# Performance work log

Measured on AMD Instinct MI355X. Metric: run time of the kernel, lower is better.

The kernel has to match this reference:

```python
import jax, jax.numpy as jnp
import numpy as np
from jax import lax

BETA = 0.5
ITERATIONS = 20
EPS = 1e-12


def setup_inputs() -> dict:
    key = jax.random.key(0)
    n, K = 32768, 512
    # C plays the role of a cosine-similarity matrix; randn keeps exp(C/beta) bounded.
    C = jax.random.normal(key, (n, K), dtype=jnp.float32)
    return {"C": C}


def reference(C):
    n, K = C.shape
    a = jnp.float32(1.0 / n)          # uniform row marginal (scalar broadcast of a = ones(n,1)/n)
    b = jnp.float32(1.0 / K)          # uniform column marginal
    K_mat = jnp.exp(C / BETA)         # [n, K]
    Q0 = jnp.full((n, K), 1.0 / (n * K), dtype=C.dtype)
    sigma0 = jnp.full((K,), 1.0 / K, dtype=C.dtype)

    def step(carry, _):
        Q, sigma = carry
        Q = K_mat * sigma[None, :]                              # elementwise column scaling
        Q = Q / (jnp.sum(Q, axis=1, keepdims=True) + EPS) * a   # row-normalize to marginal a
        sigma = b / (jnp.sum(Q, axis=0) + EPS)                  # column sums (== Q^T @ ones)
        return (Q, sigma), None

    (Q, sigma), _ = lax.scan(step, (Q0, sigma0), None, length=ITERATIONS)
    return Q * n
```

## Files before the change

kernel.cpp:

```cpp
#include <hip/hip_runtime.h>
#include <cmath>


namespace {
constexpr int ROWS = 32768;
constexpr int COLS = 512;
constexpr int ITERS = 20;
constexpr float EPS = 1e-12f;
constexpr float A_M = 1.0f / 32768.0f;
constexpr float B_M = 1.0f / 512.0f;
constexpr float L2E2 = 2.8853900817779268f;
constexpr int NSH = 8;
constexpr int SLAB_ROWS = ROWS / 8;
constexpr int GSIG_OFF = 0;
constexpr int TSUM_OFF = ITERS * COLS;
constexpr int FLAG_OFF = TSUM_OFF + (ITERS - 1) * NSH * COLS;
constexpr size_t KB_BYTES = (size_t)ROWS * COLS * 2;
constexpr size_t CTRL_FLOATS = (size_t)FLAG_OFF + 512;
constexpr int PBLK = 512;
constexpr int PRPW = 8;
constexpr int WPB = 4;
constexpr int MID_BLOCKS = 1024;
constexpr int MID_RPW = 8;
constexpr int BIG_BLOCKS = 2048;
constexpr int BIG_RPW = 4;

typedef float f4v __attribute__((ext_vector_type(4)));
}

__device__ __forceinline__ float bflo(unsigned u) {
  union { unsigned i; float f; } v; v.i = u << 16; return v.f;
}
__device__ __forceinline__ float bfhi(unsigned u) {
  union { unsigned i; float f; } v; v.i = u & 0xFFFF0000u; return v.f;
}
__device__ __forceinline__ unsigned f2bf(float f) {
  union { float f; unsigned u; } v; v.f = f;
  return (v.u + 0x7FFFu + ((v.u >> 16) & 1u)) >> 16;
}
__device__ __forceinline__ int row_base_mid(int bid, int wave) {
  return (bid & 7) * SLAB_ROWS + ((bid >> 3) * WPB + wave) * MID_RPW;
}
__device__ __forceinline__ int row_base_big(int bid, int wave) {
  return (bid & 7) * SLAB_ROWS + ((bid >> 3) * WPB + wave) * BIG_RPW;
}

__global__ __launch_bounds__(256) void ipot_zero_kernel(float* __restrict__ ctrl) {
  const size_t stride = (size_t)gridDim.x * blockDim.x;
  const size_t gtid = (size_t)blockIdx.x * blockDim.x + threadIdx.x;
  if (gtid < COLS) ctrl[GSIG_OFF + gtid] = B_M;
  const size_t zsz = (size_t)(ITERS - 1) * NSH * COLS + 512;
  for (size_t i = gtid; i < zsz; i += stride) ctrl[TSUM_OFF + i] = 0.0f;
}

__global__ __launch_bounds__(512, 4) void ipot_persist_kernel(
    const float* __restrict__ C, float* __restrict__ out,
    float* __restrict__ ctrl) {
  __shared__ float sig[COLS];
  __shared__ float part[8][COLS];
  const int tid = threadIdx.x;
  const int wave = tid >> 6;
  const int lane = tid & 63;
  const int slab = blockIdx.x & 7;
  const size_t row0 = ((size_t)blockIdx.x * 8 + wave) * PRPW;
  unsigned* flags = (unsigned*)(ctrl + FLAG_OFF);

  unsigned kb[PRPW][4];
  {
    const float* rp = C + row0 * COLS + 8 * lane;
    f4v c0 = __builtin_nontemporal_load((const f4v*)rp);
    f4v c1 = __builtin_nontemporal_load((const f4v*)(rp + 4));
#pragma unroll
    for (int r = 0; r < PRPW; ++r) {
      f4v d0 = c0, d1 = c1;
      if (r + 1 < PRPW) {
        const float* np = rp + (size_t)(r + 1) * COLS;
        c0 = __builtin_nontemporal_load((const f4v*)np);
        c1 = __builtin_nontemporal_load((const f4v*)(np + 4));
      }
      d0.x = exp2f(d0.x * L2E2); d0.y = exp2f(d0.y * L2E2);
      d0.z = exp2f(d0.z * L2E2); d0.w = exp2f(d0.w * L2E2);
      d1.x = exp2f(d1.x * L2E2); d1.y = exp2f(d1.y * L2E2);
      d1.z = exp2f(d1.z * L2E2); d1.w = exp2f(d1.w * L2E2);
      kb[r][0] = f2bf(d0.x) | (f2bf(d0.y) << 16);
      kb[r][1] = f2bf(d0.z) | (f2bf(d0.w) << 16);
      kb[r][2] = f2bf(d1.x) | (f2bf(d1.y) << 16);
      kb[r][3] = f2bf(d1.z) | (f2bf(d1.w) << 16);
    }
  }
  sig[tid] = B_M;
  __syncthreads();

  for (int t = 0; t < ITERS - 1; ++t) {
    const float4 sA = *(const float4*)&sig[8 * lane];
    const float4 sB = *(const float4*)&sig[8 * lane + 4];
    float p[PRPW];
#pragma unroll
    for (int r = 0; r < PRPW; ++r) {
      p[r] = bflo(kb[r][0]) * sA.x + bfhi(kb[r][0]) * sA.y +
             bflo(kb[r][1]) * sA.z + bfhi(kb[r][1]) * sA.w +
             bflo(kb[r][2]) * sB.x + bfhi(kb[r][2]) * sB.y +
             bflo(kb[r][3]) * sB.z + bfhi(kb[r][3]) * sB.w;
    }
#pragma unroll
    for (int off = 32; off; off >>= 1) {
#pragma unroll
      for (int r = 0; r < PRPW; ++r) p[r] += __shfl_xor(p[r], off, 64);
    }
    float a[8] = {0.f, 0.f, 0.f, 0.f, 0.f, 0.f, 0.f, 0.f};
#pragma unroll
    for (int r = 0; r < PRPW; ++r) {
      const float inv = 1.0f / (p[r] + EPS);
      a[0] += bflo(kb[r][0]) * inv; a[1] += bfhi(kb[r][0]) * inv;
      a[2] += bflo(kb[r][1]) * inv; a[3] += bfhi(kb[r][1]) * inv;
      a[4] += bflo(kb[r][2]) * inv; a[5] += bfhi(kb[r][2]) * inv;
      a[6] += bflo(kb[r][3]) * inv; a[7] += bfhi(kb[r][3]) * inv;
    }
    *(float4*)&part[wave][8 * lane] = *(float4*)&a[0];
    *(float4*)&part[wave][8 * lane + 4] = *(float4*)&a[4];
    __syncthreads();

    {
      float v = part[0][tid] + part[1][tid] + part[2][tid] + part[3][tid] +
                part[4][tid] + part[5][tid] + part[6][tid] + part[7][tid];
      float* ts = ctrl + TSUM_OFF + ((size_t)t * NSH + slab) * COLS;
      atomicAdd(&ts[tid], v);
    }

    __syncthreads();
    if (tid == 0)
      __hip_atomic_store(&flags[blockIdx.x], (unsigned)(t + 1),
                         __ATOMIC_RELAXED, __HIP_MEMORY_SCOPE_AGENT);
    while (__hip_atomic_load(&flags[tid], __ATOMIC_RELAXED,
                             __HIP_MEMORY_SCOPE_AGENT) < (unsigned)(t + 1))
      __builtin_amdgcn_s_sleep(1);
    __syncthreads();
    __builtin_amdgcn_fence(__ATOMIC_ACQUIRE, "agent");

    const float* tb = ctrl + TSUM_OFF + (size_t)t * NSH * COLS;
    float T = 0.f;
#pragma unroll
    for (int s = 0; s < NSH; ++s)
      T += __hip_atomic_load(&tb[s * COLS + tid], __ATOMIC_RELAXED,
                             __HIP_MEMORY_SCOPE_AGENT);
    sig[tid] = B_M / (sig[tid] * A_M * T + EPS);
    __syncthreads();
  }

  {
    const float4 sA = *(const float4*)&sig[8 * lane];
    const float4 sB = *(const float4*)&sig[8 * lane + 4];
    float p[PRPW];
#pragma unroll
    for (int r = 0; r < PRPW; ++r) {
      p[r] = bflo(kb[r][0]) * sA.x + bfhi(kb[r][0]) * sA.y +
             bflo(kb[r][1]) * sA.z + bfhi(kb[r][1]) * sA.w +
             bflo(kb[r][2]) * sB.x + bfhi(kb[r][2]) * sB.y +
             bflo(kb[r][3]) * sB.z + bfhi(kb[r][3]) * sB.w;
    }
#pragma unroll
    for (int off = 32; off; off >>= 1) {
#pragma unroll
      for (int r = 0; r < PRPW; ++r) p[r] += __shfl_xor(p[r], off, 64);
    }
#pragma unroll
    for (int r = 0; r < PRPW; ++r) {
      const float inv = 1.0f / (p[r] + EPS);
      float* wp = out + (row0 + r) * COLS + 8 * lane;
      f4v o0, o1;
      o0.x = bflo(kb[r][0]) * sA.x * inv; o0.y = bfhi(kb[r][0]) * sA.y * inv;
      o0.z = bflo(kb[r][1]) * sA.z * inv; o0.w = bfhi(kb[r][1]) * sA.w * inv;
      o1.x = bflo(kb[r][2]) * sB.x * inv; o1.y = bfhi(kb[r][2]) * sB.y * inv;
      o1.z = bflo(kb[r][3]) * sB.z * inv; o1.w = bfhi(kb[r][3]) * sB.w * inv;
      __builtin_nontemporal_store(o0, (f4v*)wp);
      __builtin_nontemporal_store(o1, (f4v*)(wp + 4));
    }
  }
}

template <bool NT_C>
__global__ __launch_bounds__(256, 8) void ipot_pass0_kernel(
    const float* __restrict__ C, unsigned short* __restrict__ Kb,
    float* __restrict__ ctrl) {
  __shared__ float part[WPB][COLS];
  const int tid = threadIdx.x;
  const int wave = tid >> 6;
  const int lane = tid & 63;
  const int wrow = row_base_big(blockIdx.x, wave);

  f4v c0[BIG_RPW], c1[BIG_RPW];
#pragma unroll
  for (int r = 0; r < BIG_RPW; ++r) {
    const f4v* rp = (const f4v*)(C + (size_t)(wrow + r) * COLS);
    if (NT_C) {
      c0[r] = __builtin_nontemporal_load(&rp[2 * lane]);
      c1[r] = __builtin_nontemporal_load(&rp[2 * lane + 1]);
    } else {
      c0[r] = rp[2 * lane];
      c1[r] = rp[2 * lane + 1];
    }
  }
  float p[BIG_RPW];
#pragma unroll
  for (int r = 0; r < BIG_RPW; ++r) {
    c0[r].x = exp2f(c0[r].x * L2E2); c0[r].y = exp2f(c0[r].y * L2E2);
    c0[r].z = exp2f(c0[r].z * L2E2); c0[r].w = exp2f(c0[r].w * L2E2);
    c1[r].x = exp2f(c1[r].x * L2E2); c1[r].y = exp2f(c1[r].y * L2E2);
    c1[r].z = exp2f(c1[r].z * L2E2); c1[r].w = exp2f(c1[r].w * L2E2);
    uint4 kp;
    kp.x = f2bf(c0[r].x) | (f2bf(c0[r].y) << 16);
    kp.y = f2bf(c0[r].z) | (f2bf(c0[r].w) << 16);
    kp.z = f2bf(c1[r].x) | (f2bf(c1[r].y) << 16);
    kp.w = f2bf(c1[r].z) | (f2bf(c1[r].w) << 16);
    ((uint4*)(Kb + (size_t)(wrow + r) * COLS))[lane] = kp;
    p[r] = ((c0[r].x + c0[r].y) + (c0[r].z + c0[r].w)) +
           ((c1[r].x + c1[r].y) + (c1[r].z + c1[r].w));
  }
#pragma unroll
  for (int off = 32; off; off >>= 1) {
#pragma unroll
    for (int r = 0; r < BIG_RPW; ++r) p[r] += __shfl_xor(p[r], off, 64);
  }
  float a[8] = {0.f, 0.f, 0.f, 0.f, 0.f, 0.f, 0.f, 0.f};
#pragma unroll
  for (int r = 0; r < BIG_RPW; ++r) {
    const float inv = 1.0f / (B_M * p[r] + EPS);
    a[0] += c0[r].x * inv; a[1] += c0[r].y * inv;
    a[2] += c0[r].z * inv; a[3] += c0[r].w * inv;
    a[4] += c1[r].x * inv; a[5] += c1[r].y * inv;
    a[6] += c1[r].z * inv; a[7] += c1[r].w * inv;
  }
  *(float4*)&part[wave][8 * lane] = *(float4*)&a[0];
  *(float4*)&part[wave][8 * lane + 4] = *(float4*)&a[4];
  __syncthreads();
  float* ts = ctrl + TSUM_OFF + (size_t)(blockIdx.x & 7) * COLS;
  int j = tid;
  atomicAdd(&ts[j], part[0][j] + part[1][j] + part[2][j] + part[3][j]);
  j += 256;
  atomicAdd(&ts[j], part[0][j] + part[1][j] + part[2][j] + part[3][j]);
}

__global__ __launch_bounds__(256, 4) void ipot_mid_kernel(
    const unsigned short* __restrict__ Kb, float* __restrict__ ctrl, int t) {
  __shared__ float sig[COLS];
  __shared__ float part[WPB][COLS];
  const int tid = threadIdx.x;
  const int wave = tid >> 6;
  const int lane = tid & 63;
  const int wrow = row_base_mid(blockIdx.x, wave);

  const float* gsp = ctrl + GSIG_OFF + (size_t)(t - 1) * COLS;
  const float* tb = ctrl + TSUM_OFF + (size_t)(t - 1) * NSH * COLS;
  float tv0[NSH], tv1[NSH];
#pragma unroll
  for (int s = 0; s < NSH; ++s) {
    tv0[s] = tb[s * COLS + tid];
    tv1[s] = tb[s * COLS + tid + 256];
  }
  const float g0 = gsp[tid];
  const float g1 = gsp[tid + 256];

  uint4 kr[MID_RPW];
#pragma unroll
  for (int r = 0; r < MID_RPW; ++r)
    kr[r] = ((const uint4*)(Kb + (size_t)(wrow + r) * COLS))[lane];
  {
    float T0 = 0.f, T1 = 0.f;
#pragma unroll
    for (int s = 0; s < NSH; ++s) { T0 += tv0[s]; T1 += tv1[s]; }
    const float sv0 = B_M / (g0 * A_M * T0 + EPS);
    const float sv1 = B_M / (g1 * A_M * T1 + EPS);
    sig[tid] = sv0;
    sig[tid + 256] = sv1;
    if (blockIdx.x == 0) {
      float* gsc = ctrl + GSIG_OFF + (size_t)t * COLS;
      gsc[tid] = sv0;
      gsc[tid + 256] = sv1;
    }
  }
  __syncthreads();

  const float4 sA = *(const float4*)&sig[8 * lane];
  const float4 sB = *(const float4*)&sig[8 * lane + 4];
  float p[MID_RPW];
#pragma unroll
  for (int r = 0; r < MID_RPW; ++r) {
    p[r] = bflo(kr[r].x) * sA.x + bfhi(kr[r].x) * sA.y +
           bflo(kr[r].y) * sA.z + bfhi(kr[r].y) * sA.w +
           bflo(kr[r].z) * sB.x + bfhi(kr[r].z) * sB.y +
           bflo(kr[r].w) * sB.z + bfhi(kr[r].w) * sB.w;
  }
#pragma unroll
  for (int off = 32; off; off >>= 1) {
#pragma unroll
    for (int r = 0; r < MID_RPW; ++r) p[r] += __shfl_xor(p[r], off, 64);
  }
  float a[8] = {0.f, 0.f, 0.f, 0.f, 0.f, 0.f, 0.f, 0.f};
#pragma unroll
  for (int r = 0; r < MID_RPW; ++r) {
    const float inv = 1.0f / (p[r] + EPS);
    a[0] += bflo(kr[r].x) * inv; a[1] += bfhi(kr[r].x) * inv;
    a[2] += bflo(kr[r].y) * inv; a[3] += bfhi(kr[r].y) * inv;
    a[4] += bflo(kr[r].z) * inv; a[5] += bfhi(kr[r].z) * inv;
    a[6] += bflo(kr[r].w) * inv; a[7] += bfhi(kr[r].w) * inv;
  }
  *(float4*)&part[wave][8 * lane] = *(float4*)&a[0];
  *(float4*)&part[wave][8 * lane + 4] = *(float4*)&a[4];
  __syncthreads();
  float* ts = ctrl + TSUM_OFF + ((size_t)t * NSH + (blockIdx.x & 7)) * COLS;
  int j = tid;
  atomicAdd(&ts[j], part[0][j] + part[1][j] + part[2][j] + part[3][j]);
  j += 256;
  atomicAdd(&ts[j], part[0][j] + part[1][j] + part[2][j] + part[3][j]);
}

__global__ __launch_bounds__(256, 8) void ipot_final_kb_kernel(
    const unsigned short* __restrict__ Kb, float* __restrict__ out,
    const float* __restrict__ ctrl) {
  __shared__ float sig[COLS];
  const int tid = threadIdx.x;
  const int wave = tid >> 6;
  const int lane = tid & 63;
  const int wrow = row_base_big(blockIdx.x, wave);

  const int t = ITERS - 1;
  const float* gsp = ctrl + GSIG_OFF + (size_t)(t - 1) * COLS;
  const float* tb = ctrl + TSUM_OFF + (size_t)(t - 1) * NSH * COLS;
  float tv0[NSH], tv1[NSH];
#pragma unroll
  for (int s = 0; s < NSH; ++s) {
    tv0[s] = tb[s * COLS + tid];
    tv1[s] = tb[s * COLS + tid + 256];
  }
  const float g0 = gsp[tid];
  const float g1 = gsp[tid + 256];

  uint4 kr[BIG_RPW];
#pragma unroll
  for (int r = 0; r < BIG_RPW; ++r)
    kr[r] = ((const uint4*)(Kb + (size_t)(wrow + r) * COLS))[lane];
  {
    float T0 = 0.f, T1 = 0.f;
#pragma unroll
    for (int s = 0; s < NSH; ++s) { T0 += tv0[s]; T1 += tv1[s]; }
    sig[tid] = B_M / (g0 * A_M * T0 + EPS);
    sig[tid + 256] = B_M / (g1 * A_M * T1 + EPS);
  }
  __syncthreads();

  const float4 sA = *(const float4*)&sig[8 * lane];
  const float4 sB = *(const float4*)&sig[8 * lane + 4];
  float p[BIG_RPW];
#pragma unroll
  for (int r = 0; r < BIG_RPW; ++r) {
    p[r] = bflo(kr[r].x) * sA.x + bfhi(kr[r].x) * sA.y +
           bflo(kr[r].y) * sA.z + bfhi(kr[r].y) * sA.w +
           bflo(kr[r].z) * sB.x + bfhi(kr[r].z) * sB.y +
           bflo(kr[r].w) * sB.z + bfhi(kr[r].w) * sB.w;
  }
#pragma unroll
  for (int off = 32; off; off >>= 1) {
#pragma unroll
    for (int r = 0; r < BIG_RPW; ++r) p[r] += __shfl_xor(p[r], off, 64);
  }
#pragma unroll
  for (int r = 0; r < BIG_RPW; ++r) {
    const float inv = 1.0f / (p[r] + EPS);
    f4v* wp = (f4v*)(out + (size_t)(wrow + r) * COLS);
    f4v o0, o1;
    o0.x = bflo(kr[r].x) * sA.x * inv; o0.y = bfhi(kr[r].x) * sA.y * inv;
    o0.z = bflo(kr[r].y) * sA.z * inv; o0.w = bfhi(kr[r].y) * sA.w * inv;
    o1.x = bflo(kr[r].z) * sB.x * inv; o1.y = bfhi(kr[r].z) * sB.y * inv;
    o1.z = bflo(kr[r].w) * sB.z * inv; o1.w = bfhi(kr[r].w) * sB.w * inv;
    __builtin_nontemporal_store(o0, &wp[2 * lane]);
    __builtin_nontemporal_store(o1, &wp[2 * lane + 1]);
  }
}

extern "C" void kernel_launch(void* const* d_in, const int* in_sizes, int n_in,
                              void* d_out, int out_size, void* d_ws, size_t ws_size,
                              hipStream_t stream) {
  const float* C = (const float*)d_in[0];
  float* out = (float*)d_out;
  unsigned short* Kb = (unsigned short*)d_ws;
  float* ctrl = (float*)((char*)d_ws + KB_BYTES);
  const bool ws_ok = ws_size >= KB_BYTES + CTRL_FLOATS * sizeof(float);
  if (!ws_ok) ctrl = (float*)d_ws;

  ipot_zero_kernel<<<128, 256, 0, stream>>>(ctrl);

  int occ = 0;
  hipError_t oe = hipOccupancyMaxActiveBlocksPerMultiprocessor(
      &occ, reinterpret_cast<const void*>(&ipot_persist_kernel), 512, 0);
  bool persist = ws_ok && (oe == hipSuccess) && (occ >= 2);
  if (persist) {
    void* args[] = {(void*)&C, (void*)&out, (void*)&ctrl};
    hipError_t ce = hipLaunchCooperativeKernel(
        reinterpret_cast<void*>(&ipot_persist_kernel), dim3(PBLK), dim3(512),
        args, 0, stream);
    if (ce != hipSuccess) persist = false;
  }
  if (!persist) {
    ipot_pass0_kernel<true><<<BIG_BLOCKS, 256, 0, stream>>>(C, Kb, ctrl);
    for (int t = 1; t < ITERS - 1; ++t)
      ipot_mid_kernel<<<MID_BLOCKS, 256, 0, stream>>>(Kb, ctrl, t);
    ipot_final_kb_kernel<<<BIG_BLOCKS, 256, 0, stream>>>(Kb, out, ctrl);
  }
}
```

Before: 185.4 us.

## Use 256 blocks of 1024 threads with 32 sum shadows in persistent kernel

The persistent cooperative kernel now runs 256 blocks of 1024 threads (16 waves each, one block per CU) instead of 512 blocks of 512 threads. This halves the number of flags each grid barrier must poll, and a single wave polls them with a wave-wide all-check. Column-sum atomics are spread over 32 shadow copies instead of 8 to reduce atomic contention. Per-block reduction now sums 16 wave partials, and the reader sums 32 shadows per column each iteration. The risks are lower occupancy per CU and extra reads per sync.

Measured after the change: 185.0 us. About the same (-0.2%).

```diff
diff --git a/kernel.cpp b/kernel.cpp
--- a/kernel.cpp
+++ b/kernel.cpp
@@ -10,20 +10,22 @@
 constexpr float A_M = 1.0f / 32768.0f;
 constexpr float B_M = 1.0f / 512.0f;
 constexpr float L2E2 = 2.8853900817779268f;
-constexpr int NSH = 8;
-constexpr int SLAB_ROWS = ROWS / 8;
 constexpr int GSIG_OFF = 0;
 constexpr int TSUM_OFF = ITERS * COLS;
-constexpr int FLAG_OFF = TSUM_OFF + (ITERS - 1) * NSH * COLS;
+constexpr int NSHP = 32;
+constexpr int FLAG_OFF = TSUM_OFF + (ITERS - 1) * NSHP * COLS;
 constexpr size_t KB_BYTES = (size_t)ROWS * COLS * 2;
-constexpr size_t CTRL_FLOATS = (size_t)FLAG_OFF + 512;
-constexpr int PBLK = 512;
+constexpr size_t CTRL_FLOATS = (size_t)FLAG_OFF + 256;
+constexpr int PBLK = 256;
+constexpr int PWAVES = 16;
 constexpr int PRPW = 8;
+constexpr int NSHF = 8;
 constexpr int WPB = 4;
 constexpr int MID_BLOCKS = 1024;
 constexpr int MID_RPW = 8;
 constexpr int BIG_BLOCKS = 2048;
 constexpr int BIG_RPW = 4;
+constexpr int SLAB_ROWS = ROWS / 8;
 
 typedef float f4v __attribute__((ext_vector_type(4)));
 }
@@ -49,20 +51,20 @@
   const size_t stride = (size_t)gridDim.x * blockDim.x;
   const size_t gtid = (size_t)blockIdx.x * blockDim.x + threadIdx.x;
   if (gtid < COLS) ctrl[GSIG_OFF + gtid] = B_M;
-  const size_t zsz = (size_t)(ITERS - 1) * NSH * COLS + 512;
+  const size_t zsz = (size_t)(ITERS - 1) * NSHP * COLS + 256;
   for (size_t i = gtid; i < zsz; i += stride) ctrl[TSUM_OFF + i] = 0.0f;
 }
 
-__global__ __launch_bounds__(512, 4) void ipot_persist_kernel(
+__global__ __launch_bounds__(1024, 4) void ipot_persist_kernel(
     const float* __restrict__ C, float* __restrict__ out,
     float* __restrict__ ctrl) {
   __shared__ float sig[COLS];
-  __shared__ float part[8][COLS];
+  __shared__ float part[PWAVES][COLS];
   const int tid = threadIdx.x;
   const int wave = tid >> 6;
   const int lane = tid & 63;
-  const int slab = blockIdx.x & 7;
-  const size_t row0 = ((size_t)blockIdx.x * 8 + wave) * PRPW;
+  const int shadow = blockIdx.x & (NSHP - 1);
+  const size_t row0 = ((size_t)blockIdx.x * PWAVES + wave) * PRPW;
   unsigned* flags = (unsigned*)(ctrl + FLAG_OFF);
 
   unsigned kb[PRPW][4];
@@ -88,7 +90,7 @@
       kb[r][3] = f2bf(d1.z) | (f2bf(d1.w) << 16);
     }
   }
-  sig[tid] = B_M;
+  if (tid < COLS) sig[tid] = B_M;
   __syncthreads();
 
   for (int t = 0; t < ITERS - 1; ++t) {
@@ -120,10 +122,11 @@
     *(float4*)&part[wave][8 * lane + 4] = *(float4*)&a[4];
     __syncthreads();
 
-    {
-      float v = part[0][tid] + part[1][tid] + part[2][tid] + part[3][tid] +
-                part[4][tid] + part[5][tid] + part[6][tid] + part[7][tid];
-      float* ts = ctrl + TSUM_OFF + ((size_t)t * NSH + slab) * COLS;
+    if (tid < COLS) {
+      float v = 0.f;
+#pragma unroll
+      for (int w = 0; w < PWAVES; ++w) v += part[w][tid];
+      float* ts = ctrl + TSUM_OFF + ((size_t)t * NSHP + shadow) * COLS;
       atomicAdd(&ts[tid], v);
     }
 
@@ -131,19 +134,34 @@
     if (tid == 0)
       __hip_atomic_store(&flags[blockIdx.x], (unsigned)(t + 1),
                          __ATOMIC_RELAXED, __HIP_MEMORY_SCOPE_AGENT);
-    while (__hip_atomic_load(&flags[tid], __ATOMIC_RELAXED,
-                             __HIP_MEMORY_SCOPE_AGENT) < (unsigned)(t + 1))
-      __builtin_amdgcn_s_sleep(1);
+    if (wave == 0) {
+      const unsigned want = (unsigned)(t + 1);
+      for (;;) {
+        unsigned m0 = __hip_atomic_load(&flags[lane], __ATOMIC_RELAXED,
+                                        __HIP_MEMORY_SCOPE_AGENT);
+        unsigned m1 = __hip_atomic_load(&flags[lane + 64], __ATOMIC_RELAXED,
+                                        __HIP_MEMORY_SCOPE_AGENT);
+        unsigned m2 = __hip_atomic_load(&flags[lane + 128], __ATOMIC_RELAXED,
+                                        __HIP_MEMORY_SCOPE_AGENT);
+        unsigned m3 = __hip_atomic_load(&flags[lane + 192], __ATOMIC_RELAXED,
+                                        __HIP_MEMORY_SCOPE_AGENT);
+        unsigned mn = min(min(m0, m1), min(m2, m3));
+        if (__all(mn >= want)) break;
+        __builtin_amdgcn_s_sleep(1);
+      }
+    }
     __syncthreads();
     __builtin_amdgcn_fence(__ATOMIC_ACQUIRE, "agent");
 
-    const float* tb = ctrl + TSUM_OFF + (size_t)t * NSH * COLS;
-    float T = 0.f;
-#pragma unroll
-    for (int s = 0; s < NSH; ++s)
-      T += __hip_atomic_load(&tb[s * COLS + tid], __ATOMIC_RELAXED,
-                             __HIP_MEMORY_SCOPE_AGENT);
-    sig[tid] = B_M / (sig[tid] * A_M * T + EPS);
+    if (tid < COLS) {
+      const float* tb = ctrl + TSUM_OFF + (size_t)t * NSHP * COLS;
+      float T = 0.f;
+#pragma unroll
+      for (int s = 0; s < NSHP; ++s)
+        T += __hip_atomic_load(&tb[s * COLS + tid], __ATOMIC_RELAXED,
+                               __HIP_MEMORY_SCOPE_AGENT);
+      sig[tid] = B_M / (sig[tid] * A_M * T + EPS);
+    }
     __syncthreads();
   }
 
@@ -250,10 +268,10 @@
   const int wrow = row_base_mid(blockIdx.x, wave);
 
   const float* gsp = ctrl + GSIG_OFF + (size_t)(t - 1) * COLS;
-  const float* tb = ctrl + TSUM_OFF + (size_t)(t - 1) * NSH * COLS;
-  float tv0[NSH], tv1[NSH];
-#pragma unroll
-  for (int s = 0; s < NSH; ++s) {
+  const float* tb = ctrl + TSUM_OFF + (size_t)(t - 1) * NSHF * COLS;
+  float tv0[NSHF], tv1[NSHF];
+#pragma unroll
+  for (int s = 0; s < NSHF; ++s) {
     tv0[s] = tb[s * COLS + tid];
     tv1[s] = tb[s * COLS + tid + 256];
   }
@@ -267,7 +285,7 @@
   {
     float T0 = 0.f, T1 = 0.f;
 #pragma unroll
-    for (int s = 0; s < NSH; ++s) { T0 += tv0[s]; T1 += tv1[s]; }
+    for (int s = 0; s < NSHF; ++s) { T0 += tv0[s]; T1 += tv1[s]; }
     const float sv0 = B_M / (g0 * A_M * T0 + EPS);
     const float sv1 = B_M / (g1 * A_M * T1 + EPS);
     sig[tid] = sv0;
@@ -307,7 +325,7 @@
   *(float4*)&part[wave][8 * lane] = *(float4*)&a[0];
   *(float4*)&part[wave][8 * lane + 4] = *(float4*)&a[4];
   __syncthreads();
-  float* ts = ctrl + TSUM_OFF + ((size_t)t * NSH + (blockIdx.x & 7)) * COLS;
+  float* ts = ctrl + TSUM_OFF + ((size_t)t * NSHF + (blockIdx.x & 7)) * COLS;
   int j = tid;
   atomicAdd(&ts[j], part[0][j] + part[1][j] + part[2][j] + part[3][j]);
   j += 256;
@@ -325,10 +343,10 @@
 
   const int t = ITERS - 1;
   const float* gsp = ctrl + GSIG_OFF + (size_t)(t - 1) * COLS;
-  const float* tb = ctrl + TSUM_OFF + (size_t)(t - 1) * NSH * COLS;
-  float tv0[NSH], tv1[NSH];
-#pragma unroll
-  for (int s = 0; s < NSH; ++s) {
+  const float* tb = ctrl + TSUM_OFF + (size_t)(t - 1) * NSHF * COLS;
+  float tv0[NSHF], tv1[NSHF];
+#pragma unroll
+  for (int s = 0; s < NSHF; ++s) {
     tv0[s] = tb[s * COLS + tid];
     tv1[s] = tb[s * COLS + tid + 256];
   }
@@ -342,7 +360,7 @@
   {
     float T0 = 0.f, T1 = 0.f;
 #pragma unroll
-    for (int s = 0; s < NSH; ++s) { T0 += tv0[s]; T1 += tv1[s]; }
+    for (int s = 0; s < NSHF; ++s) { T0 += tv0[s]; T1 += tv1[s]; }
     sig[tid] = B_M / (g0 * A_M * T0 + EPS);
     sig[tid + 256] = B_M / (g1 * A_M * T1 + EPS);
   }
@@ -387,16 +405,16 @@
   const bool ws_ok = ws_size >= KB_BYTES + CTRL_FLOATS * sizeof(float);
   if (!ws_ok) ctrl = (float*)d_ws;
 
-  ipot_zero_kernel<<<128, 256, 0, stream>>>(ctrl);
+  ipot_zero_kernel<<<256, 256, 0, stream>>>(ctrl);
 
   int occ = 0;
   hipError_t oe = hipOccupancyMaxActiveBlocksPerMultiprocessor(
-      &occ, reinterpret_cast<const void*>(&ipot_persist_kernel), 512, 0);
-  bool persist = ws_ok && (oe == hipSuccess) && (occ >= 2);
+      &occ, reinterpret_cast<const void*>(&ipot_persist_kernel), 1024, 0);
+  bool persist = ws_ok && (oe == hipSuccess) && (occ >= 1);
   if (persist) {
     void* args[] = {(void*)&C, (void*)&out, (void*)&ctrl};
     hipError_t ce = hipLaunchCooperativeKernel(
-        reinterpret_cast<void*>(&ipot_persist_kernel), dim3(PBLK), dim3(512),
+        reinterpret_cast<void*>(&ipot_persist_kernel), dim3(PBLK), dim3(1024),
         args, 0, stream);
     if (ce != hipSuccess) persist = false;
   }
```
